# Performance work log

Hardware: AMD Instinct MI355X
Metric: run time of the kernel (lower is better)

Reference implementation:

```python
import jax, jax.numpy as jnp
import numpy as np

B_SZ, N_INST, D_IN, D_OUT, C_COMP, M_RANK = 512, 4, 1024, 1024, 64, 256

def setup_inputs() -> dict:
    key = jax.random.key(0)
    k1, k2, k3, k4 = jax.random.split(key, 4)
    x = jax.random.normal(k1, (B_SZ, N_INST, D_IN), dtype=jnp.float32)
    A = jax.random.normal(k2, (N_INST, C_COMP, D_IN, M_RANK), dtype=jnp.float32) * 0.02
    Bp = jax.random.normal(k3, (N_INST, C_COMP, M_RANK, D_OUT), dtype=jnp.float32) * 0.02
    topk_mask = jax.random.randint(k4, (B_SZ, N_INST, C_COMP), 0, 2, dtype=jnp.int32)
    return {"x": x, "A": A, "B": Bp, "topk_mask": topk_mask}

def reference(x, A, B, topk_mask):
    # inner: [b, i, C, m]
    inner = jnp.einsum('bid,icdm->bicm', x, A)
    inner = inner * topk_mask.astype(inner.dtype)[..., None]
    # comp: [b, i, C, d_out]
    comp = jnp.einsum('bicm,icmo->bico', inner, B)
    # sum over components C -> [b, i, d_out]
    return comp.sum(axis=2)
```

## Files before the change

### kernel.cpp

```cpp
#include <hip/hip_runtime.h>
#include <hip/hip_bf16.h>
#include <stdint.h>

#define B_SZ   512
#define NINST  4
#define D_IN   1024
#define D_OUTD 1024
#define CCOMP  64
#define MRANK  256
#define KTOT   (CCOMP*MRANK)

typedef __attribute__((ext_vector_type(4))) float  f32x4;
typedef __attribute__((ext_vector_type(8))) __bf16 bf16x8;
typedef __attribute__((ext_vector_type(4))) __bf16 bf16x4;

__device__ inline void gload16(const void* g, void* l) {
  __builtin_amdgcn_global_load_lds(
      (const __attribute__((address_space(1))) void*)g,
      (__attribute__((address_space(3))) void*)l, 16, 0, 0);
}

#define BARN(N) do { \
  asm volatile("s_waitcnt lgkmcnt(0) vmcnt(" #N ")" ::: "memory"); \
  __builtin_amdgcn_sched_barrier(0); \
  __builtin_amdgcn_s_barrier(); \
  __builtin_amdgcn_sched_barrier(0); } while (0)

__global__ __launch_bounds__(256)
void xcvt_kernel(const float* __restrict__ x, __bf16* __restrict__ xbf)
{
  const int total = (B_SZ*NINST*D_IN) / 4;
  for (int v = blockIdx.x*256 + threadIdx.x; v < total; v += gridDim.x*256) {
    const int k4 = v & 255;
    const int i  = (v >> 8) & 3;
    const int b  = v >> 10;
    f32x4 f = ((const f32x4*)x)[v];
    bf16x4 h; h[0]=(__bf16)f.x; h[1]=(__bf16)f.y; h[2]=(__bf16)f.z; h[3]=(__bf16)f.w;
    ((bf16x4*)xbf)[((size_t)i*B_SZ + b)*256 + k4] = h;
  }
}

__global__ __launch_bounds__(256, 2)
void p1_kernel(const __bf16* __restrict__ xbf, const float* __restrict__ A,
               const int* __restrict__ mask, __bf16* __restrict__ inner)
{
  const int bid = blockIdx.x;
  const int L   = (bid & 7) * 64 + (bid >> 3);
  const int bt  = L & 3;
  const int mt  = (L >> 2) & 1;
  const int icg = L >> 3;
  const int ic0 = icg * 4;
  const int i   = ic0 >> 6;
  const int c0  = ic0 & 63;
  const int b0  = bt * 128;
  const int m0  = mt * 128;

  const int tid  = threadIdx.x;
  const int lane = tid & 63;
  const int wid  = tid >> 6;
  const int wr   = wid >> 1;
  const int wc   = wid & 1;

  __shared__ __align__(16) char smem[65536];
  __bf16* Xs = (__bf16*)smem;
  __bf16* As = (__bf16*)(smem + 32768);

  f32x4 acc[4][4];
#pragma unroll
  for (int a_ = 0; a_ < 4; ++a_)
#pragma unroll
    for (int b_ = 0; b_ < 4; ++b_)
      acc[a_][b_] = (f32x4){0.f, 0.f, 0.f, 0.f};

  const __bf16* xbase  = xbf + ((size_t)i * B_SZ + b0) * D_IN;
  const float*  Abase0 = A + (size_t)ic0 * D_IN * MRANK + m0;

  const int bo = tid & 127;
  const int bg = tid >> 7;
  float areg[4][8];

  auto stageXs = [&](int buf, int kt) {
#pragma unroll
    for (int q = 0; q < 4; ++q) {
      const int ci  = wid*4 + q;
      const int row = ci*8 + (lane >> 3);
      const int kch = (lane & 7) ^ (row & 7);
      gload16(xbase + (size_t)row * D_IN + (kt & 15)*64 + kch*8,
              Xs + buf*8192 + ci*512);
    }
  };
  auto loadA = [&](int kt) {
    const float* Ab = Abase0 + (size_t)(kt >> 4) * D_IN * MRANK;
#pragma unroll
    for (int q = 0; q < 4; ++q)
#pragma unroll
      for (int j = 0; j < 8; ++j)
        areg[q][j] = Ab[(size_t)((kt & 15)*64 + (bg*4+q)*8 + j)*MRANK + bo];
  };
  auto writeA = [&](int buf) {
#pragma unroll
    for (int q = 0; q < 4; ++q) {
      const int oct = bg*4 + q;
      bf16x8 h;
#pragma unroll
      for (int j = 0; j < 8; ++j) h[j] = (__bf16)areg[q][j];
      *(bf16x8*)(As + buf*8192 + bo*64 + ((oct ^ (bo & 7)))*8) = h;
    }
  };

  stageXs(0, 0); loadA(0); writeA(0);
  __syncthreads();

  int cur = 0;
  for (int kt = 0; kt < 64; ++kt) {
    if (kt+1 < 64) { stageXs(cur ^ 1, kt+1); loadA(kt+1); }
#pragma unroll
    for (int kk = 0; kk < 2; ++kk) {
      const int oct = kk*4 + (lane >> 4);
      bf16x8 af[4];
#pragma unroll
      for (int mi = 0; mi < 4; ++mi) {
        const int row = wr*64 + mi*16 + (lane & 15);
        af[mi] = *(const bf16x8*)(Xs + cur*8192 + row*64 + ((oct ^ (row & 7)))*8);
      }
#pragma unroll
      for (int ni = 0; ni < 4; ++ni) {
        const int col = wc*64 + ni*16 + (lane & 15);
        bf16x8 bfr = *(const bf16x8*)(As + cur*8192 + col*64 + ((oct ^ (col & 7)))*8);
#pragma unroll
        for (int mi = 0; mi < 4; ++mi)
          acc[mi][ni] = __builtin_amdgcn_mfma_f32_16x16x32_bf16(af[mi], bfr, acc[mi][ni], 0, 0, 0);
      }
    }
    if ((kt & 15) == 15) {
      const int c = c0 + (kt >> 4);
      __bf16* obase = inner + ((size_t)i * B_SZ + b0) * KTOT + (size_t)c * MRANK + m0;
      float mv[16];
#pragma unroll
      for (int mi = 0; mi < 4; ++mi)
#pragma unroll
        for (int j = 0; j < 4; ++j) {
          const int row = wr*64 + mi*16 + (lane >> 4)*4 + j;
          mv[mi*4+j] = (float)mask[(size_t)(b0 + row) * (NINST*CCOMP) + i*CCOMP + c];
        }
#pragma unroll
      for (int mi = 0; mi < 4; ++mi)
#pragma unroll
        for (int ni = 0; ni < 4; ++ni) {
          const int colL = wc*64 + ni*16 + (lane & 15);
#pragma unroll
          for (int j = 0; j < 4; ++j) {
            const int rowL = wr*64 + mi*16 + (lane >> 4)*4 + j;
            obase[(size_t)rowL * KTOT + colL] = (__bf16)(acc[mi][ni][j] * mv[mi*4+j]);
          }
#pragma unroll
          for (int j = 0; j < 4; ++j) acc[mi][ni][j] = 0.f;
        }
    }
    if (kt+1 < 64) writeA(cur ^ 1);
    __syncthreads();
    cur ^= 1;
  }
}

__global__ __launch_bounds__(512, 1)
void p2_kernel(const __bf16* __restrict__ inner, const float* __restrict__ Bm,
               float* __restrict__ dst, int nks)
{
  const int bid = blockIdx.x;
  const int nwg = gridDim.x;
  const int L   = (bid & 7) * (nwg >> 3) + (bid >> 3);
  const int tile = L & 7;
  const int rest = L >> 3;
  const int ks  = rest % nks;
  const int i   = rest / nks;
  const int mt  = tile & 1;
  const int nt  = tile >> 1;
  const int b0  = mt * 256;
  const int o0  = nt * 256;
  const int NSTEP = (KTOT/64) / nks;
  const int kb0   = ks * NSTEP;

  const int tid  = threadIdx.x;
  const int lane = tid & 63;
  const int wid  = tid >> 6;
  const int wr   = wid >> 2;
  const int wc   = wid & 3;

  __shared__ __align__(16) char smem[163840];
  __bf16* As = (__bf16*)smem;
  __bf16* Bs = (__bf16*)(smem + 98304);

  f32x4 acc[8][4];
#pragma unroll
  for (int a_ = 0; a_ < 8; ++a_)
#pragma unroll
    for (int b_ = 0; b_ < 4; ++b_)
      acc[a_][b_] = (f32x4){0.f, 0.f, 0.f, 0.f};

  const __bf16* ibase = inner + ((size_t)i * B_SZ + b0) * KTOT;
  const float*  Bbase = Bm + (size_t)i * KTOT * D_OUTD + o0;

  const int bo = tid & 255;
  const int bg = tid >> 8;
  float breg[4][8];

  auto stageA = [&](int slot, int kt) {
#pragma unroll
    for (int q = 0; q < 4; ++q) {
      const int u   = wid*4 + q;
      const int row = u*8 + (lane >> 3);
      const int kch = (lane & 7) ^ (row & 7);
      gload16(ibase + (size_t)row * KTOT + (size_t)(kb0 + kt)*64 + kch*8,
              As + slot*16384 + u*512);
    }
  };
  auto loadB = [&](int kt) {
#pragma unroll
    for (int q = 0; q < 4; ++q)
#pragma unroll
      for (int j = 0; j < 8; ++j)
        breg[q][j] = Bbase[(size_t)((size_t)(kb0 + kt)*64 + (bg*4+q)*8 + j)*D_OUTD + bo];
  };
  auto writeB = [&](int buf) {
#pragma unroll
    for (int q = 0; q < 4; ++q) {
      const int oct = bg*4 + q;
      bf16x8 h;
#pragma unroll
      for (int j = 0; j < 8; ++j) h[j] = (__bf16)breg[q][j];
      *(bf16x8*)(Bs + buf*16384 + bo*64 + ((oct ^ (bo & 7)))*8) = h;
    }
  };

  stageA(0, 0);
  stageA(1, 1);
  loadB(0); writeB(0);
  BARN(0);

  for (int t = 0; t < NSTEP; ++t) {
    const int aslot = t % 3;
    const int bbuf  = t & 1;
    if (t+2 < NSTEP) stageA((t+2) % 3, t+2);
    if (t+1 < NSTEP) loadB(t+1);
#pragma unroll
    for (int kk = 0; kk < 2; ++kk) {
      const int oct = kk*4 + (lane >> 4);
      bf16x8 bf[4];
#pragma unroll
      for (int ni = 0; ni < 4; ++ni) {
        const int col = wc*64 + ni*16 + (lane & 15);
        bf[ni] = *(const bf16x8*)(Bs + bbuf*16384 + col*64 + ((oct ^ (col & 7)))*8);
      }
#pragma unroll
      for (int mh = 0; mh < 2; ++mh) {
        bf16x8 af[4];
#pragma unroll
        for (int mi = 0; mi < 4; ++mi) {
          const int row = wr*128 + (mh*4 + mi)*16 + (lane & 15);
          af[mi] = *(const bf16x8*)(As + aslot*16384 + row*64 + ((oct ^ (row & 7)))*8);
        }
        __builtin_amdgcn_s_setprio(1);
#pragma unroll
        for (int ni = 0; ni < 4; ++ni)
#pragma unroll
          for (int mi = 0; mi < 4; ++mi)
            acc[mh*4+mi][ni] = __builtin_amdgcn_mfma_f32_16x16x32_bf16(
                af[mi], bf[ni], acc[mh*4+mi][ni], 0, 0, 0);
        __builtin_amdgcn_s_setprio(0);
      }
    }
    if (t+1 < NSTEP) writeB(bbuf ^ 1);
    if (t+2 < NSTEP) BARN(4);
    else             BARN(0);
  }

  float* obase = dst + (size_t)ks * ((size_t)B_SZ*NINST*D_OUTD)
               + ((size_t)b0 * NINST + i) * D_OUTD + o0;
#pragma unroll
  for (int mi = 0; mi < 8; ++mi)
#pragma unroll
    for (int ni = 0; ni < 4; ++ni) {
      const int colL = wc*64 + ni*16 + (lane & 15);
#pragma unroll
      for (int j = 0; j < 4; ++j) {
        const int rowL = wr*128 + mi*16 + (lane >> 4)*4 + j;
        obase[(size_t)rowL * (NINST*D_OUTD) + colL] = acc[mi][ni][j];
      }
    }
}

__global__ __launch_bounds__(256)
void reduce_kernel(const float* __restrict__ part, float* __restrict__ out, int nks)
{
  const int total = (B_SZ*NINST*D_OUTD) / 4;
  for (int v = blockIdx.x*256 + threadIdx.x; v < total; v += gridDim.x*256) {
    f32x4 s = ((const f32x4*)part)[v];
    for (int ks = 1; ks < nks; ++ks)
      s += ((const f32x4*)part)[(size_t)ks*total + v];
    ((f32x4*)out)[v] = s;
  }
}

extern "C" void kernel_launch(void* const* d_in, const int* in_sizes, int n_in,
                              void* d_out, int out_size, void* d_ws, size_t ws_size,
                              hipStream_t stream) {
  const float* x    = (const float*)d_in[0];
  const float* A    = (const float*)d_in[1];
  const float* Bm   = (const float*)d_in[2];
  const int*   mask = (const int*)d_in[3];

  const size_t innerB = (size_t)NINST * B_SZ * KTOT * 2;
  const size_t xbfB   = (size_t)NINST * B_SZ * D_IN * 2;
  const size_t partB  = (size_t)B_SZ * NINST * D_OUTD * 4;

  char* p = (char*)d_ws;
  __bf16* inner = (__bf16*)p;             p += innerB;
  __bf16* xbf   = (__bf16*)p;             p += xbfB;
  const size_t used = (size_t)(p - (char*)d_ws);

  int nks = 1;
  if      (ws_size >= used + 8*partB) nks = 8;
  else if (ws_size >= used + 4*partB) nks = 4;
  else if (ws_size >= used + 2*partB) nks = 2;
  float* part = (nks > 1) ? (float*)p : (float*)d_out;

  xcvt_kernel<<<dim3(1024),  dim3(256), 0, stream>>>(x, xbf);
  p1_kernel<<<dim3(512),     dim3(256), 0, stream>>>(xbf, A, mask, inner);
  p2_kernel<<<dim3(32*nks),  dim3(512), 0, stream>>>(inner, Bm, part, nks);
  if (nks > 1)
    reduce_kernel<<<dim3(1024), dim3(256), 0, stream>>>(part, (float*)d_out, nks);
}
```

Baseline: 259.2 us.

## Enlarge p1 GEMM tile to 256x256 with 512 threads and triple-buffered X staging

Restructures the first-phase kernel to use 512-thread blocks that compute a full 256-row by 256-rank tile over two components, in place of 128x128 tiles over four components. X is staged through a three-slot async LDS ring and A through double buffering, with partial vmcnt waits, matching the p2 kernel's pipeline. The goal is to halve redundant A reads and conversions per output and to overlap global loads with MFMA. It also reorders p2's prologue so the B load is issued first and relaxes its barrier waits. In exchange it uses 160KB of LDS and more accumulator registers per thread, and launches only 256 blocks.

Result: slower. 442.6 us (+70.8%).

```diff
diff --git a/kernel.cpp b/kernel.cpp
--- a/kernel.cpp
+++ b/kernel.cpp
@@ -40,53 +40,52 @@
   }
 }
 
-__global__ __launch_bounds__(256, 2)
+__global__ __launch_bounds__(512, 1)
 void p1_kernel(const __bf16* __restrict__ xbf, const float* __restrict__ A,
                const int* __restrict__ mask, __bf16* __restrict__ inner)
 {
   const int bid = blockIdx.x;
-  const int L   = (bid & 7) * 64 + (bid >> 3);
-  const int bt  = L & 3;
-  const int mt  = (L >> 2) & 1;
-  const int icg = L >> 3;
-  const int ic0 = icg * 4;
+  const int L   = (bid & 7) * 32 + (bid >> 3);
+  const int bt  = L & 1;
+  const int icg = L >> 1;
+  const int ic0 = icg * 2;
   const int i   = ic0 >> 6;
   const int c0  = ic0 & 63;
-  const int b0  = bt * 128;
-  const int m0  = mt * 128;
+  const int b0  = bt * 256;
+  const int NSTEP = 32;
 
   const int tid  = threadIdx.x;
   const int lane = tid & 63;
   const int wid  = tid >> 6;
-  const int wr   = wid >> 1;
-  const int wc   = wid & 1;
-
-  __shared__ __align__(16) char smem[65536];
+  const int wr   = wid >> 2;
+  const int wc   = wid & 3;
+
+  __shared__ __align__(16) char smem[163840];
   __bf16* Xs = (__bf16*)smem;
-  __bf16* As = (__bf16*)(smem + 32768);
-
-  f32x4 acc[4][4];
-#pragma unroll
-  for (int a_ = 0; a_ < 4; ++a_)
+  __bf16* As = (__bf16*)(smem + 98304);
+
+  f32x4 acc[8][4];
+#pragma unroll
+  for (int a_ = 0; a_ < 8; ++a_)
 #pragma unroll
     for (int b_ = 0; b_ < 4; ++b_)
       acc[a_][b_] = (f32x4){0.f, 0.f, 0.f, 0.f};
 
   const __bf16* xbase  = xbf + ((size_t)i * B_SZ + b0) * D_IN;
-  const float*  Abase0 = A + (size_t)ic0 * D_IN * MRANK + m0;
-
-  const int bo = tid & 127;
-  const int bg = tid >> 7;
+  const float*  Abase0 = A + (size_t)ic0 * D_IN * MRANK;
+
+  const int bo = tid & 255;
+  const int bg = tid >> 8;
   float areg[4][8];
 
-  auto stageXs = [&](int buf, int kt) {
+  auto stageX = [&](int slot, int kt) {
 #pragma unroll
     for (int q = 0; q < 4; ++q) {
-      const int ci  = wid*4 + q;
-      const int row = ci*8 + (lane >> 3);
+      const int u   = wid*4 + q;
+      const int row = u*8 + (lane >> 3);
       const int kch = (lane & 7) ^ (row & 7);
       gload16(xbase + (size_t)row * D_IN + (kt & 15)*64 + kch*8,
-              Xs + buf*8192 + ci*512);
+              Xs + slot*16384 + u*512);
     }
   };
   auto loadA = [&](int kt) {
@@ -104,62 +103,78 @@
       bf16x8 h;
 #pragma unroll
       for (int j = 0; j < 8; ++j) h[j] = (__bf16)areg[q][j];
-      *(bf16x8*)(As + buf*8192 + bo*64 + ((oct ^ (bo & 7)))*8) = h;
-    }
-  };
-
-  stageXs(0, 0); loadA(0); writeA(0);
-  __syncthreads();
-
-  int cur = 0;
-  for (int kt = 0; kt < 64; ++kt) {
-    if (kt+1 < 64) { stageXs(cur ^ 1, kt+1); loadA(kt+1); }
+      *(bf16x8*)(As + buf*16384 + bo*64 + ((oct ^ (bo & 7)))*8) = h;
+    }
+  };
+  auto computeStep = [&](int slot, int buf) {
 #pragma unroll
     for (int kk = 0; kk < 2; ++kk) {
       const int oct = kk*4 + (lane >> 4);
-      bf16x8 af[4];
-#pragma unroll
-      for (int mi = 0; mi < 4; ++mi) {
-        const int row = wr*64 + mi*16 + (lane & 15);
-        af[mi] = *(const bf16x8*)(Xs + cur*8192 + row*64 + ((oct ^ (row & 7)))*8);
-      }
+      bf16x8 bf[4];
 #pragma unroll
       for (int ni = 0; ni < 4; ++ni) {
         const int col = wc*64 + ni*16 + (lane & 15);
-        bf16x8 bfr = *(const bf16x8*)(As + cur*8192 + col*64 + ((oct ^ (col & 7)))*8);
-#pragma unroll
-        for (int mi = 0; mi < 4; ++mi)
-          acc[mi][ni] = __builtin_amdgcn_mfma_f32_16x16x32_bf16(af[mi], bfr, acc[mi][ni], 0, 0, 0);
-      }
-    }
-    if ((kt & 15) == 15) {
-      const int c = c0 + (kt >> 4);
-      __bf16* obase = inner + ((size_t)i * B_SZ + b0) * KTOT + (size_t)c * MRANK + m0;
-      float mv[16];
-#pragma unroll
-      for (int mi = 0; mi < 4; ++mi)
+        bf[ni] = *(const bf16x8*)(As + buf*16384 + col*64 + ((oct ^ (col & 7)))*8);
+      }
+#pragma unroll
+      for (int mh = 0; mh < 2; ++mh) {
+        bf16x8 af[4];
+#pragma unroll
+        for (int mi = 0; mi < 4; ++mi) {
+          const int row = wr*128 + (mh*4 + mi)*16 + (lane & 15);
+          af[mi] = *(const bf16x8*)(Xs + slot*16384 + row*64 + ((oct ^ (row & 7)))*8);
+        }
+        __builtin_amdgcn_s_setprio(1);
+#pragma unroll
+        for (int ni = 0; ni < 4; ++ni)
+#pragma unroll
+          for (int mi = 0; mi < 4; ++mi)
+            acc[mh*4+mi][ni] = __builtin_amdgcn_mfma_f32_16x16x32_bf16(
+                af[mi], bf[ni], acc[mh*4+mi][ni], 0, 0, 0);
+        __builtin_amdgcn_s_setprio(0);
+      }
+    }
+  };
+  auto segEpilogue = [&](int t) {
+    const int c = c0 + (t >> 4);
+    __bf16* obase = inner + ((size_t)i * B_SZ + b0) * KTOT + (size_t)c * MRANK;
+#pragma unroll
+    for (int mi = 0; mi < 8; ++mi) {
+      float mv[4];
+#pragma unroll
+      for (int j = 0; j < 4; ++j) {
+        const int row = wr*128 + mi*16 + (lane >> 4)*4 + j;
+        mv[j] = (float)mask[(size_t)(b0 + row) * (NINST*CCOMP) + i*CCOMP + c];
+      }
+#pragma unroll
+      for (int ni = 0; ni < 4; ++ni) {
+        const int colL = wc*64 + ni*16 + (lane & 15);
 #pragma unroll
         for (int j = 0; j < 4; ++j) {
-          const int row = wr*64 + mi*16 + (lane >> 4)*4 + j;
-          mv[mi*4+j] = (float)mask[(size_t)(b0 + row) * (NINST*CCOMP) + i*CCOMP + c];
+          const int rowL = wr*128 + mi*16 + (lane >> 4)*4 + j;
+          obase[(size_t)rowL * KTOT + colL] = (__bf16)(acc[mi][ni][j] * mv[j]);
         }
 #pragma unroll
-      for (int mi = 0; mi < 4; ++mi)
-#pragma unroll
-        for (int ni = 0; ni < 4; ++ni) {
-          const int colL = wc*64 + ni*16 + (lane & 15);
-#pragma unroll
-          for (int j = 0; j < 4; ++j) {
-            const int rowL = wr*64 + mi*16 + (lane >> 4)*4 + j;
-            obase[(size_t)rowL * KTOT + colL] = (__bf16)(acc[mi][ni][j] * mv[mi*4+j]);
-          }
-#pragma unroll
-          for (int j = 0; j < 4; ++j) acc[mi][ni][j] = 0.f;
-        }
-    }
-    if (kt+1 < 64) writeA(cur ^ 1);
-    __syncthreads();
-    cur ^= 1;
+        for (int j = 0; j < 4; ++j) acc[mi][ni][j] = 0.f;
+      }
+    }
+  };
+
+  loadA(0);
+  stageX(0, 0);
+  stageX(1, 1);
+  writeA(0);
+  BARN(4);
+
+  for (int t = 0; t < NSTEP; ++t) {
+    const int slot = t % 3;
+    const int buf  = t & 1;
+    if (t+1 < NSTEP) loadA(t+1);
+    if (t+2 < NSTEP) stageX((t+2) % 3, t+2);
+    computeStep(slot, buf);
+    if (t+1 < NSTEP) writeA(buf ^ 1);
+    if ((t & 15) == 15) segEpilogue(t);
+    if ((t & 15) == 15 || t >= NSTEP-2) BARN(0); else BARN(4);
   }
 }
 
@@ -233,16 +248,17 @@
     }
   };
 
+  loadB(0);
   stageA(0, 0);
   stageA(1, 1);
-  loadB(0); writeB(0);
-  BARN(0);
+  writeB(0);
+  BARN(4);
 
   for (int t = 0; t < NSTEP; ++t) {
     const int aslot = t % 3;
     const int bbuf  = t & 1;
+    if (t+1 < NSTEP) loadB(t+1);
     if (t+2 < NSTEP) stageA((t+2) % 3, t+2);
-    if (t+1 < NSTEP) loadB(t+1);
 #pragma unroll
     for (int kk = 0; kk < 2; ++kk) {
       const int oct = kk*4 + (lane >> 4);
@@ -271,8 +287,7 @@
       }
     }
     if (t+1 < NSTEP) writeB(bbuf ^ 1);
-    if (t+2 < NSTEP) BARN(4);
-    else             BARN(0);
+    if (t >= NSTEP-2) BARN(0); else BARN(4);
   }
 
   float* obase = dst + (size_t)ks * ((size_t)B_SZ*NINST*D_OUTD)
@@ -326,7 +341,7 @@
   float* part = (nks > 1) ? (float*)p : (float*)d_out;
 
   xcvt_kernel<<<dim3(1024),  dim3(256), 0, stream>>>(x, xbf);
-  p1_kernel<<<dim3(512),     dim3(256), 0, stream>>>(xbf, A, mask, inner);
+  p1_kernel<<<dim3(256),     dim3(512), 0, stream>>>(xbf, A, mask, inner);
   p2_kernel<<<dim3(32*nks),  dim3(512), 0, stream>>>(inner, Bm, part, nks);
   if (nks > 1)
     reduce_kernel<<<dim3(1024), dim3(256), 0, stream>>>(part, (float*)d_out, nks);
```
